# Performance work log

Measured on AMD Instinct MI355X. Metric: run time of the kernel, lower is better.

## Reference

```python
import jax, jax.numpy as jnp
import numpy as np

N, E, C, H0, H1 = 100_000, 1_600_000, 32, 128, 64


def _sage(x, src, dst, wl, bl, wr, n):
    # PyG SAGEConv(aggr='min'): lin_l(min_{j in N(i)} x_j) + lin_r(x_i); lin_r has no bias.
    agg = jax.ops.segment_min(x[src], dst, num_segments=n)  # [n, d]
    # nodes with no in-edges: PyG fills with 0 (segment_min yields dtype max)
    agg = jnp.where(agg >= jnp.finfo(x.dtype).max, jnp.zeros((), x.dtype), agg)
    return agg @ wl + bl + x @ wr


def _bn(x, g, b, eps=1e-5):
    # training-mode BatchNorm over the node dimension
    mu = jnp.mean(x, axis=0)
    var = jnp.var(x, axis=0)
    return (x - mu) * jax.lax.rsqrt(var + eps) * g + b


def _forward(x, edge_index,
             rm1_wl, rm1_bl, rm1_wr, rmn1_g, rmn1_b,
             rm2_wl, rm2_bl, rm2_wr, rmn2_g, rmn2_b,
             rm4_wl, rm4_bl, rm4_wr,
             sh1_wl, sh1_bl, sh1_wr, shn1_g, shn1_b,
             rt1_wl, rt1_bl, rt1_wr, rtn1_g, rtn1_b, rt3_w, rt3_b,
             md1_wl, md1_bl, md1_wr, mdn1_g, mdn1_b, md3_w, md3_b):
    n = x.shape[0]
    src, dst = edge_index[0], edge_index[1]
    rm = jax.nn.relu(_bn(_sage(x, src, dst, rm1_wl, rm1_bl, rm1_wr, n), rmn1_g, rmn1_b))
    rm = jax.nn.relu(_bn(_sage(rm, src, dst, rm2_wl, rm2_bl, rm2_wr, n), rmn2_g, rmn2_b))
    rm = _sage(rm, src, dst, rm4_wl, rm4_bl, rm4_wr, n)  # [n, 3]
    xs = jnp.concatenate([x, rm], axis=1)  # [n, C+3]
    xs = jax.nn.relu(_bn(_sage(xs, src, dst, sh1_wl, sh1_bl, sh1_wr, n), shn1_g, shn1_b))
    rm_ls = jax.nn.log_softmax(rm, axis=1)
    labels = (jnp.argmax(rm_ls, axis=1) == 2).astype(x.dtype)  # [n]
    rt = jax.nn.relu(_bn(_sage(xs, src, dst, rt1_wl, rt1_bl, rt1_wr, n), rtn1_g, rtn1_b))
    rt = (rt @ rt3_w + rt3_b).ravel() * labels
    md = jax.nn.relu(_bn(_sage(xs, src, dst, md1_wl, md1_bl, md1_wr, n), mdn1_g, mdn1_b))
    md = (md @ md3_w + md3_b).ravel() * labels
    return rm_ls, rt, md


def setup_inputs() -> dict:
    key = jax.random.key(0)
    ks = iter(jax.random.split(key, 64))

    def w(shape):
        s = 1.0 / np.sqrt(shape[0])
        return jax.random.uniform(next(ks), shape, jnp.float32, -s, s)

    inp = {
        "x": jax.random.normal(next(ks), (N, C), jnp.float32),
        "edge_index": jax.random.randint(next(ks), (2, E), 0, N, dtype=jnp.int32),
    }

    def sage_params(cin, cout, name):
        inp[name + "_wl"] = w((cin, cout))
        inp[name + "_bl"] = jnp.zeros((cout,), jnp.float32)
        inp[name + "_wr"] = w((cin, cout))

    def bn_params(c, name):
        inp[name + "_g"] = jnp.ones((c,), jnp.float32)
        inp[name + "_b"] = jnp.zeros((c,), jnp.float32)

    sage_params(C, H0, "rm1"); bn_params(H0, "rmn1")
    sage_params(H0, H1, "rm2"); bn_params(H1, "rmn2")
    sage_params(H1, 3, "rm4")
    sage_params(C + 3, H0, "sh1"); bn_params(H0, "shn1")
    sage_params(H0, H1, "rt1"); bn_params(H1, "rtn1")
    inp["rt3_w"] = w((H1, 1)); inp["rt3_b"] = jnp.zeros((1,), jnp.float32)
    sage_params(H0, H1, "md1"); bn_params(H1, "mdn1")
    inp["md3_w"] = w((H1, 1)); inp["md3_b"] = jnp.zeros((1,), jnp.float32)
    return inp


def reference(x, edge_index,
              rm1_wl, rm1_bl, rm1_wr, rmn1_g, rmn1_b,
              rm2_wl, rm2_bl, rm2_wr, rmn2_g, rmn2_b,
              rm4_wl, rm4_bl, rm4_wr,
              sh1_wl, sh1_bl, sh1_wr, shn1_g, shn1_b,
              rt1_wl, rt1_bl, rt1_wr, rtn1_g, rtn1_b, rt3_w, rt3_b,
              md1_wl, md1_bl, md1_wr, mdn1_g, mdn1_b, md3_w, md3_b):
    return _forward(x, edge_index,
                    rm1_wl, rm1_bl, rm1_wr, rmn1_g, rmn1_b,
                    rm2_wl, rm2_bl, rm2_wr, rmn2_g, rmn2_b,
                    rm4_wl, rm4_bl, rm4_wr,
                    sh1_wl, sh1_bl, sh1_wr, shn1_g, shn1_b,
                    rt1_wl, rt1_bl, rt1_wr, rtn1_g, rtn1_b, rt3_w, rt3_b,
                    md1_wl, md1_bl, md1_wr, mdn1_g, mdn1_b, md3_w, md3_b)
```

## Files before the change

### kernel.cpp

```cpp
#include <hip/hip_runtime.h>

#define FLTMAX 3.402823466e+38f
#define DEV __device__ __forceinline__

typedef unsigned short u16;
typedef unsigned int u32;
typedef __bf16 bf16_t;
typedef bf16_t bf16x8 __attribute__((ext_vector_type(8)));
typedef float f32x4 __attribute__((ext_vector_type(4)));

union U16x8 { uint4 u; bf16x8 b; };

DEV float trf(float v, float a, float b) { return fmaxf(fmaf(v, a, b), 0.f); }

DEV u16 f2bf(float f) {
    u32 u = __float_as_uint(f);
    return (u16)((u + 0x7FFFu + ((u >> 16) & 1u)) >> 16);
}

__global__ __launch_bounds__(256) void hist_k(const int* __restrict__ dst,
                                              int* __restrict__ deg, int E) {
    int e = blockIdx.x * 256 + threadIdx.x;
    if (e >= E) return;
    atomicAdd(&deg[dst[e]], 1);
}

__global__ __launch_bounds__(256) void scan_block_k(const int* __restrict__ deg,
                                                    int* __restrict__ ptr,
                                                    int* __restrict__ bsum, int n) {
    __shared__ int ls[256];
    int i = blockIdx.x * 256 + threadIdx.x;
    int v = (i < n) ? deg[i] : 0;
    ls[threadIdx.x] = v;
    __syncthreads();
#pragma unroll
    for (int off = 1; off < 256; off <<= 1) {
        int a = (threadIdx.x >= off) ? ls[threadIdx.x - off] : 0;
        __syncthreads();
        ls[threadIdx.x] += a;
        __syncthreads();
    }
    if (i < n) ptr[i] = ls[threadIdx.x] - v;
    if (threadIdx.x == 255) bsum[blockIdx.x] = ls[255];
}

__global__ __launch_bounds__(512) void scan_bsum_k(int* __restrict__ bsum, int nb) {
    __shared__ int ls[512];
    int t = threadIdx.x;
    int v = (t < nb) ? bsum[t] : 0;
    ls[t] = v;
    __syncthreads();
#pragma unroll
    for (int off = 1; off < 512; off <<= 1) {
        int a = (t >= off) ? ls[t - off] : 0;
        __syncthreads();
        ls[t] += a;
        __syncthreads();
    }
    if (t < nb) bsum[t] = ls[t] - v;
}

__global__ __launch_bounds__(256) void scan_add_k(int* __restrict__ ptr,
                                                  int* __restrict__ pos,
                                                  const int* __restrict__ bsum,
                                                  int n, int E) {
    int i = blockIdx.x * 256 + threadIdx.x;
    if (i == 0) ptr[n] = E;
    if (i < n) {
        int p = ptr[i] + bsum[blockIdx.x];
        ptr[i] = p;
        pos[i] = p;
    }
}

__global__ __launch_bounds__(256) void csr_fill_part_k(
    const int* __restrict__ src, const int* __restrict__ dst,
    int* __restrict__ pos, int* __restrict__ csr, int E, int lo_step) {
    const int part = blockIdx.x & 7;
    const int e = (blockIdx.x >> 3) * 256 + threadIdx.x;
    if (e >= E) return;
    const int d = dst[e];
    const int lo = part * lo_step;
    const int hi = lo + lo_step;
    if (d < lo || d >= hi) return;
    const int p = atomicAdd(&pos[d], 1);
    csr[p] = src[e];
}

__global__ __launch_bounds__(256) void gather_min32_k(
    const float* __restrict__ feat, const int* __restrict__ ptr,
    const int* __restrict__ csr, float* __restrict__ agg, int n) {
    const int lane = threadIdx.x & 63;
    const int wave = (blockIdx.x * 256 + threadIdx.x) >> 6;
    const int node = wave * 2 + (lane >> 5);
    if (node >= n) return;
    const int fl = lane & 31;
    int e = ptr[node];
    const int end = ptr[node + 1];
    const bool empty = (e == end);
    float m = FLTMAX;
    for (; e + 7 < end; e += 8) {
        int s[8];
#pragma unroll
        for (int j = 0; j < 8; j++) s[j] = csr[e + j];
        float v[8];
#pragma unroll
        for (int j = 0; j < 8; j++) v[j] = feat[(size_t)s[j] * 32 + fl];
#pragma unroll
        for (int j = 0; j < 8; j++) m = fminf(m, v[j]);
    }
    for (; e < end; e++) m = fminf(m, feat[(size_t)csr[e] * 32 + fl]);
    agg[(size_t)node * 32 + fl] = empty ? 0.f : m;
}

__global__ __launch_bounds__(256) void gather_min128_k(
    const float* __restrict__ feat, const int* __restrict__ ptr,
    const int* __restrict__ csr, const float* __restrict__ coef,
    float* __restrict__ agg, int n) {
    const int lane = threadIdx.x & 63;
    const int node = (blockIdx.x * 256 + threadIdx.x) >> 6;
    if (node >= n) return;
    const int fl = lane * 2;
    const float ca0 = coef[fl], ca1 = coef[fl + 1];
    const float cb0 = coef[128 + fl], cb1 = coef[128 + fl + 1];
    int e = ptr[node];
    const int end = ptr[node + 1];
    const bool empty = (e == end);
    float m0 = FLTMAX, m1 = FLTMAX;
    for (; e + 7 < end; e += 8) {
        int s[8];
#pragma unroll
        for (int j = 0; j < 8; j++) s[j] = csr[e + j];
        float2 v[8];
#pragma unroll
        for (int j = 0; j < 8; j++) v[j] = *(const float2*)(feat + (size_t)s[j] * 128 + fl);
#pragma unroll
        for (int j = 0; j < 8; j++) {
            m0 = fminf(m0, trf(v[j].x, ca0, cb0));
            m1 = fminf(m1, trf(v[j].y, ca1, cb1));
        }
    }
    for (; e + 3 < end; e += 4) {
        int s[4];
#pragma unroll
        for (int j = 0; j < 4; j++) s[j] = csr[e + j];
        float2 v[4];
#pragma unroll
        for (int j = 0; j < 4; j++) v[j] = *(const float2*)(feat + (size_t)s[j] * 128 + fl);
#pragma unroll
        for (int j = 0; j < 4; j++) {
            m0 = fminf(m0, trf(v[j].x, ca0, cb0));
            m1 = fminf(m1, trf(v[j].y, ca1, cb1));
        }
    }
    for (; e < end; e++) {
        const float2 v = *(const float2*)(feat + (size_t)csr[e] * 128 + fl);
        m0 = fminf(m0, trf(v.x, ca0, cb0));
        m1 = fminf(m1, trf(v.y, ca1, cb1));
    }
    float2 o;
    o.x = empty ? 0.f : m0;
    o.y = empty ? 0.f : m1;
    *(float2*)(agg + (size_t)node * 128 + fl) = o;
}

__global__ __launch_bounds__(256) void gather_bf_k(
    u16* __restrict__ Acat, const int* __restrict__ ptr,
    const int* __restrict__ csr, int n) {
    const int lane = threadIdx.x & 63;
    const int node = (blockIdx.x * 256 + threadIdx.x) >> 6;
    if (node >= n) return;
    const int fl = lane * 2;
    int e = ptr[node];
    const int end = ptr[node + 1];
    u32 outv = 0;
    if (e != end) {
        float m0 = FLTMAX, m1 = FLTMAX;
        for (; e + 15 < end; e += 16) {
            int s[16];
#pragma unroll
            for (int j = 0; j < 16; j++) s[j] = csr[e + j];
            u32 v[16];
#pragma unroll
            for (int j = 0; j < 16; j++) v[j] = *(const u32*)(Acat + (size_t)s[j] * 256 + 128 + fl);
#pragma unroll
            for (int j = 0; j < 16; j++) {
                m0 = fminf(m0, __uint_as_float(v[j] << 16));
                m1 = fminf(m1, __uint_as_float(v[j] & 0xffff0000u));
            }
        }
        for (; e + 3 < end; e += 4) {
            int s[4];
#pragma unroll
            for (int j = 0; j < 4; j++) s[j] = csr[e + j];
            u32 v[4];
#pragma unroll
            for (int j = 0; j < 4; j++) v[j] = *(const u32*)(Acat + (size_t)s[j] * 256 + 128 + fl);
#pragma unroll
            for (int j = 0; j < 4; j++) {
                m0 = fminf(m0, __uint_as_float(v[j] << 16));
                m1 = fminf(m1, __uint_as_float(v[j] & 0xffff0000u));
            }
        }
        for (; e < end; e++) {
            u32 v = *(const u32*)(Acat + (size_t)csr[e] * 256 + 128 + fl);
            m0 = fminf(m0, __uint_as_float(v << 16));
            m1 = fminf(m1, __uint_as_float(v & 0xffff0000u));
        }
        outv = (__float_as_uint(m0) >> 16) | (__float_as_uint(m1) & 0xffff0000u);
    }
    *(u32*)(Acat + (size_t)node * 256 + fl) = outv;
}

__global__ __launch_bounds__(256) void gather_min3_k(
    const float* __restrict__ feat, const int* __restrict__ ptr,
    const int* __restrict__ csr, float* __restrict__ agg, int n) {
    int i = blockIdx.x * 256 + threadIdx.x;
    if (i >= n) return;
    int e = ptr[i], end = ptr[i + 1];
    bool empty = (e == end);
    float m0 = FLTMAX, m1 = FLTMAX, m2 = FLTMAX;
    for (; e < end; e++) {
        const float* r = feat + (size_t)csr[e] * 3;
        m0 = fminf(m0, r[0]);
        m1 = fminf(m1, r[1]);
        m2 = fminf(m2, r[2]);
    }
    agg[(size_t)i * 3 + 0] = empty ? 0.f : m0;
    agg[(size_t)i * 3 + 1] = empty ? 0.f : m1;
    agg[(size_t)i * 3 + 2] = empty ? 0.f : m2;
}

__global__ __launch_bounds__(256) void convert_k(
    const float* __restrict__ h, const float* __restrict__ coef,
    u16* __restrict__ Acat, int n) {
    int t = blockIdx.x * 256 + threadIdx.x;
    int total = n * 32;
    if (t >= total) return;
    int i = t >> 5;
    int dq = (t & 31) * 4;
    const float4 hv = *(const float4*)(h + (size_t)i * 128 + dq);
    const float4 ca = *(const float4*)(coef + dq);
    const float4 cb = *(const float4*)(coef + 128 + dq);
    ushort4 o;
    o.x = f2bf(trf(hv.x, ca.x, cb.x));
    o.y = f2bf(trf(hv.y, ca.y, cb.y));
    o.z = f2bf(trf(hv.z, ca.z, cb.z));
    o.w = f2bf(trf(hv.w, ca.w, cb.w));
    *(ushort4*)(Acat + (size_t)i * 256 + 128 + dq) = o;
}

__global__ __launch_bounds__(256) void wprep_k(
    const float* __restrict__ wl, const float* __restrict__ wr,
    u16* __restrict__ WT, int N) {
    int t = blockIdx.x * 256 + threadIdx.x;
    if (t >= N * 256) return;
    int c = t >> 8;
    int k = t & 255;
    float v = (k < 128) ? wl[k * N + c] : wr[(k - 128) * N + c];
    WT[(size_t)c * 256 + k] = f2bf(v);
}

__global__ __launch_bounds__(256) void gemm_bf_k(
    const u16* __restrict__ A, const u16* __restrict__ WT,
    const float* __restrict__ bl1, const float* __restrict__ bl2,
    float* __restrict__ out, int n) {
    constexpr int NT = 8;
    const int tid = threadIdx.x;
    const int wave = tid >> 6, lane = tid & 63;
    const int quad = lane >> 4, l16 = lane & 15;
    const int row0 = blockIdx.x * 64 + wave * 16;
    const int rowA = min(row0 + l16, n - 1);
    const uint4* Arow = (const uint4*)(A + (size_t)rowA * 256) + quad;

    bf16x8 a[8];
#pragma unroll
    for (int kc = 0; kc < 8; kc++) {
        U16x8 u; u.u = Arow[kc * 4];
        a[kc] = u.b;
    }
    f32x4 acc[NT];
#pragma unroll
    for (int i = 0; i < NT; i++) acc[i] = (f32x4){0.f, 0.f, 0.f, 0.f};
#pragma unroll
    for (int nt = 0; nt < NT; nt++) {
        const uint4* Brow = (const uint4*)(WT + (size_t)(nt * 16 + l16) * 256) + quad;
#pragma unroll
        for (int kc = 0; kc < 8; kc++) {
            U16x8 u; u.u = Brow[kc * 4];
            acc[nt] = __builtin_amdgcn_mfma_f32_16x16x32_bf16(a[kc], u.b, acc[nt], 0, 0, 0);
        }
    }
#pragma unroll
    for (int nt = 0; nt < NT; nt++) {
        const int col = nt * 16 + l16;
        const float bias = (col < 64) ? bl1[col] : bl2[col - 64];
#pragma unroll
        for (int r = 0; r < 4; r++) {
            const int row = row0 + quad * 4 + r;
            if (row < n) out[(size_t)row * 128 + col] = acc[nt][r] + bias;
        }
    }
}

__global__ __launch_bounds__(256) void linear1s_k(
    const float* __restrict__ agg, const float* __restrict__ h,
    const float* __restrict__ wl, const float* __restrict__ bl,
    const float* __restrict__ wr, float* __restrict__ out, int n) {
    constexpr int DOUT = 128, CT = 32, RB = 32, LDW = 36;
    __shared__ float Ash[RB * LDW];
    __shared__ float Hsh[RB * LDW];
    const int tid = threadIdx.x;
    const int base = blockIdx.x * RB;
    {
        const int sr = tid >> 3;
        const int col = (tid & 7) * 4;
        const int grow = min(base + sr, n - 1);
        *(float4*)(Ash + sr * LDW + col) = *(const float4*)(agg + (size_t)grow * 32 + col);
        *(float4*)(Hsh + sr * LDW + col) = *(const float4*)(h + (size_t)grow * 32 + col);
    }
    __syncthreads();
    const int ct = tid % CT;
    const int rt = tid / CT;
    const int col = ct * 4;
    const int row0 = base + rt * 4;
    float4 acc[4] = {};
#pragma unroll 2
    for (int k0 = 0; k0 < 32; k0 += 4) {
        float4 wlv[4], wrv[4];
#pragma unroll
        for (int j = 0; j < 4; j++) {
            wlv[j] = *(const float4*)(wl + (size_t)(k0 + j) * DOUT + col);
            wrv[j] = *(const float4*)(wr + (size_t)(k0 + j) * DOUT + col);
        }
#pragma unroll
        for (int r = 0; r < 4; r++) {
            const float4 av = *(const float4*)(Ash + (rt * 4 + r) * LDW + k0);
            const float4 hv = *(const float4*)(Hsh + (rt * 4 + r) * LDW + k0);
#pragma unroll
            for (int j = 0; j < 4; j++) {
                const float aa = j == 0 ? av.x : j == 1 ? av.y : j == 2 ? av.z : av.w;
                const float bb = j == 0 ? hv.x : j == 1 ? hv.y : j == 2 ? hv.z : hv.w;
                acc[r].x += aa * wlv[j].x + bb * wrv[j].x;
                acc[r].y += aa * wlv[j].y + bb * wrv[j].y;
                acc[r].z += aa * wlv[j].z + bb * wrv[j].z;
                acc[r].w += aa * wlv[j].w + bb * wrv[j].w;
            }
        }
    }
    const float4 bv = *(const float4*)(bl + col);
#pragma unroll
    for (int r = 0; r < 4; r++) {
        if (row0 + r < n) {
            float4 o = acc[r];
            o.x += bv.x; o.y += bv.y; o.z += bv.z; o.w += bv.w;
            *(float4*)(out + (size_t)(row0 + r) * DOUT + col) = o;
        }
    }
}

__global__ __launch_bounds__(256) void linear2_k(
    const float* __restrict__ agg, const float* __restrict__ h,
    const float* __restrict__ coef, const float* __restrict__ wl,
    const float* __restrict__ bl, const float* __restrict__ wr,
    float* __restrict__ out, int n) {
    constexpr int DIN = 128, DOUT = 64, CT = 16, RB = 64, LDW = 132;
    __shared__ float Ash[RB * LDW];
    __shared__ float Hsh[RB * LDW];
    const int tid = threadIdx.x;
    const int base = blockIdx.x * RB;
    {
        const int sr = tid >> 2;
        const int sc = tid & 3;
        const int grow = min(base + sr, n - 1);
        const float* ar = agg + (size_t)grow * DIN;
        const float* hr = h + (size_t)grow * DIN;
#pragma unroll
        for (int c = 0; c < 8; c++) {
            const int col = (sc + c * 4) * 4;
            const float4 av = *(const float4*)(ar + col);
            float4 hv = *(const float4*)(hr + col);
            const float4 ca = *(const float4*)(coef + col);
            const float4 cb = *(const float4*)(coef + DIN + col);
            hv.x = trf(hv.x, ca.x, cb.x); hv.y = trf(hv.y, ca.y, cb.y);
            hv.z = trf(hv.z, ca.z, cb.z); hv.w = trf(hv.w, ca.w, cb.w);
            *(float4*)(Ash + sr * LDW + col) = av;
            *(float4*)(Hsh + sr * LDW + col) = hv;
        }
    }
    __syncthreads();
    const int ct = tid % CT;
    const int rt = tid / CT;
    const int col = ct * 4;
    const int row0 = base + rt * 4;
    float4 acc[4] = {};
#pragma unroll 2
    for (int k0 = 0; k0 < DIN; k0 += 4) {
        float4 wlv[4], wrv[4];
#pragma unroll
        for (int j = 0; j < 4; j++) {
            wlv[j] = *(const float4*)(wl + (size_t)(k0 + j) * DOUT + col);
            wrv[j] = *(const float4*)(wr + (size_t)(k0 + j) * DOUT + col);
        }
#pragma unroll
        for (int r = 0; r < 4; r++) {
            const float4 av = *(const float4*)(Ash + (rt * 4 + r) * LDW + k0);
            const float4 hv = *(const float4*)(Hsh + (rt * 4 + r) * LDW + k0);
#pragma unroll
            for (int j = 0; j < 4; j++) {
                const float aa = j == 0 ? av.x : j == 1 ? av.y : j == 2 ? av.z : av.w;
                const float bb = j == 0 ? hv.x : j == 1 ? hv.y : j == 2 ? hv.z : hv.w;
                acc[r].x += aa * wlv[j].x + bb * wrv[j].x;
                acc[r].y += aa * wlv[j].y + bb * wrv[j].y;
                acc[r].z += aa * wlv[j].z + bb * wrv[j].z;
                acc[r].w += aa * wlv[j].w + bb * wrv[j].w;
            }
        }
    }
    const float4 bv = *(const float4*)(bl + col);
#pragma unroll
    for (int r = 0; r < 4; r++) {
        if (row0 + r < n) {
            float4 o = acc[r];
            o.x += bv.x; o.y += bv.y; o.z += bv.z; o.w += bv.w;
            *(float4*)(out + (size_t)(row0 + r) * DOUT + col) = o;
        }
    }
}

__global__ __launch_bounds__(256) void linear_shs_k(
    const float* __restrict__ aggx, const float* __restrict__ x,
    const float* __restrict__ aggr, const float* __restrict__ rm,
    const float* __restrict__ wl, const float* __restrict__ bl,
    const float* __restrict__ wr, float* __restrict__ out, int n) {
    constexpr int DOUT = 128, CT = 32, RB = 32, LDW = 36;
    __shared__ float Ash[RB * LDW];
    __shared__ float Hsh[RB * LDW];
    __shared__ float Rsh[RB * 4], Msh[RB * 4];
    const int tid = threadIdx.x;
    const int base = blockIdx.x * RB;
    {
        const int sr = tid >> 3;
        const int col = (tid & 7) * 4;
        const int grow = min(base + sr, n - 1);
        *(float4*)(Ash + sr * LDW + col) = *(const float4*)(aggx + (size_t)grow * 32 + col);
        *(float4*)(Hsh + sr * LDW + col) = *(const float4*)(x + (size_t)grow * 32 + col);
        if (tid < RB) {
            const int gr = min(base + tid, n - 1);
#pragma unroll
            for (int k = 0; k < 3; k++) {
                Rsh[tid * 4 + k] = aggr[(size_t)gr * 3 + k];
                Msh[tid * 4 + k] = rm[(size_t)gr * 3 + k];
            }
        }
    }
    __syncthreads();
    const int ct = tid % CT;
    const int rt = tid / CT;
    const int col = ct * 4;
    const int row0 = base + rt * 4;
    float4 acc[4] = {};
#pragma unroll 2
    for (int k0 = 0; k0 < 32; k0 += 4) {
        float4 wlv[4], wrv[4];
#pragma unroll
        for (int j = 0; j < 4; j++) {
            wlv[j] = *(const float4*)(wl + (size_t)(k0 + j) * DOUT + col);
            wrv[j] = *(const float4*)(wr + (size_t)(k0 + j) * DOUT + col);
        }
#pragma unroll
        for (int r = 0; r < 4; r++) {
            const float4 av = *(const float4*)(Ash + (rt * 4 + r) * LDW + k0);
            const float4 hv = *(const float4*)(Hsh + (rt * 4 + r) * LDW + k0);
#pragma unroll
            for (int j = 0; j < 4; j++) {
                const float aa = j == 0 ? av.x : j == 1 ? av.y : j == 2 ? av.z : av.w;
                const float bb = j == 0 ? hv.x : j == 1 ? hv.y : j == 2 ? hv.z : hv.w;
                acc[r].x += aa * wlv[j].x + bb * wrv[j].x;
                acc[r].y += aa * wlv[j].y + bb * wrv[j].y;
                acc[r].z += aa * wlv[j].z + bb * wrv[j].z;
                acc[r].w += aa * wlv[j].w + bb * wrv[j].w;
            }
        }
    }
#pragma unroll
    for (int k = 0; k < 3; k++) {
        const float4 wlv = *(const float4*)(wl + (size_t)(32 + k) * DOUT + col);
        const float4 wrv = *(const float4*)(wr + (size_t)(32 + k) * DOUT + col);
#pragma unroll
        for (int r = 0; r < 4; r++) {
            const float a = Rsh[(rt * 4 + r) * 4 + k];
            const float b = Msh[(rt * 4 + r) * 4 + k];
            acc[r].x += a * wlv.x + b * wrv.x;
            acc[r].y += a * wlv.y + b * wrv.y;
            acc[r].z += a * wlv.z + b * wrv.z;
            acc[r].w += a * wlv.w + b * wrv.w;
        }
    }
    const float4 bv = *(const float4*)(bl + col);
#pragma unroll
    for (int r = 0; r < 4; r++) {
        if (row0 + r < n) {
            float4 o = acc[r];
            o.x += bv.x; o.y += bv.y; o.z += bv.z; o.w += bv.w;
            *(float4*)(out + (size_t)(row0 + r) * DOUT + col) = o;
        }
    }
}

template <int D>
__global__ __launch_bounds__(256) void colstats_k(
    const float* __restrict__ x, float* __restrict__ stats, int total) {
    __shared__ float ls[256];
    int t0 = blockIdx.x * 256 + threadIdx.x;
    int stride = gridDim.x * 256;
    float s = 0.f, s2 = 0.f;
    for (int t = t0; t < total; t += stride) {
        float v = x[t];
        s += v;
        s2 += v * v;
    }
    int col = threadIdx.x % D;
    ls[threadIdx.x] = s;
    __syncthreads();
    if (threadIdx.x < D) {
        float a = s;
        for (int u = threadIdx.x + D; u < 256; u += D) a += ls[u];
        atomicAdd(&stats[col], a);
    }
    __syncthreads();
    ls[threadIdx.x] = s2;
    __syncthreads();
    if (threadIdx.x < D) {
        float a = s2;
        for (int u = threadIdx.x + D; u < 256; u += D) a += ls[u];
        atomicAdd(&stats[D + col], a);
    }
}

template <int D>
__global__ void coef_k(const float* __restrict__ stats, const float* __restrict__ g,
                       const float* __restrict__ bb, float* __restrict__ coef,
                       float invN) {
    int d = threadIdx.x;
    if (d >= D) return;
    float mu = stats[d] * invN;
    float var = stats[D + d] * invN - mu * mu;
    float a = rsqrtf(var + 1e-5f) * g[d];
    coef[d] = a;
    coef[D + d] = bb[d] - mu * a;
}

__global__ void coef_dual_k(const float* __restrict__ stats,
                            const float* __restrict__ gR, const float* __restrict__ bR,
                            const float* __restrict__ gM, const float* __restrict__ bM,
                            float* __restrict__ coefR, float* __restrict__ coefM,
                            float invN) {
    int d = threadIdx.x;
    if (d >= 128) return;
    float mu = stats[d] * invN;
    float var = stats[128 + d] * invN - mu * mu;
    bool isR = d < 64;
    int c = isR ? d : d - 64;
    float g = isR ? gR[c] : gM[c];
    float be = isR ? bR[c] : bM[c];
    float a = rsqrtf(var + 1e-5f) * g;
    float* co = isR ? coefR : coefM;
    co[c] = a;
    co[64 + c] = be - mu * a;
}

__global__ __launch_bounds__(256) void rm_fused_k(
    const float* __restrict__ h2, const float* __restrict__ coef,
    const int* __restrict__ ptr, const int* __restrict__ csr,
    const float* __restrict__ wl, const float* __restrict__ bl,
    const float* __restrict__ wr, float* __restrict__ rmb,
    float* __restrict__ ls_out, float* __restrict__ lab, int n) {
    const int lane = threadIdx.x & 63;
    const int node = (blockIdx.x * 256 + threadIdx.x) >> 6;
    if (node >= n) return;
    const float a = coef[lane], b = coef[64 + lane];
    int e = ptr[node];
    const int end = ptr[node + 1];
    const bool empty = (e == end);
    float m = FLTMAX;
    for (; e + 15 < end; e += 16) {
        int s[16];
#pragma unroll
        for (int j = 0; j < 16; j++) s[j] = csr[e + j];
        float v[16];
#pragma unroll
        for (int j = 0; j < 16; j++) v[j] = h2[(size_t)s[j] * 64 + lane];
#pragma unroll
        for (int j = 0; j < 16; j++) m = fminf(m, trf(v[j], a, b));
    }
    for (; e + 3 < end; e += 4) {
        int s[4];
#pragma unroll
        for (int j = 0; j < 4; j++) s[j] = csr[e + j];
        float v[4];
#pragma unroll
        for (int j = 0; j < 4; j++) v[j] = h2[(size_t)s[j] * 64 + lane];
#pragma unroll
        for (int j = 0; j < 4; j++) m = fminf(m, trf(v[j], a, b));
    }
    for (; e < end; e++) m = fminf(m, trf(h2[(size_t)csr[e] * 64 + lane], a, b));
    m = empty ? 0.f : m;
    const float hv = trf(h2[(size_t)node * 64 + lane], a, b);
    float c0 = m * wl[lane * 3 + 0] + hv * wr[lane * 3 + 0];
    float c1 = m * wl[lane * 3 + 1] + hv * wr[lane * 3 + 1];
    float c2 = m * wl[lane * 3 + 2] + hv * wr[lane * 3 + 2];
#pragma unroll
    for (int off = 1; off < 64; off <<= 1) {
        c0 += __shfl_xor(c0, off);
        c1 += __shfl_xor(c1, off);
        c2 += __shfl_xor(c2, off);
    }
    const float r0 = c0 + bl[0], r1 = c1 + bl[1], r2 = c2 + bl[2];
    if (lane < 3) {
        const float r = lane == 0 ? r0 : lane == 1 ? r1 : r2;
        rmb[(size_t)node * 3 + lane] = r;
        const float mx = fmaxf(r0, fmaxf(r1, r2));
        const float lse = mx + logf(expf(r0 - mx) + expf(r1 - mx) + expf(r2 - mx));
        ls_out[(size_t)node * 3 + lane] = r - lse;
        if (lane == 0) lab[node] = (r2 > r0 && r2 > r1) ? 1.f : 0.f;
    }
}

__global__ __launch_bounds__(256) void final_k(
    const float* __restrict__ rtmd,
    const float* __restrict__ cR, const float* __restrict__ cM,
    const float* __restrict__ rtw, const float* __restrict__ rtb,
    const float* __restrict__ mdw, const float* __restrict__ mdb,
    const float* __restrict__ lab, float* __restrict__ out_rt,
    float* __restrict__ out_md, int n) {
    int i = blockIdx.x * 256 + threadIdx.x;
    if (i >= n) return;
    const float* rr = rtmd + (size_t)i * 128;
    const float* mr = rr + 64;
    float a = rtb[0], b = mdb[0];
#pragma unroll 8
    for (int k = 0; k < 64; k++) {
        a += trf(rr[k], cR[k], cR[64 + k]) * rtw[k];
        b += trf(mr[k], cM[k], cM[64 + k]) * mdw[k];
    }
    float l = lab[i];
    out_rt[i] = a * l;
    out_md[i] = b * l;
}

extern "C" void kernel_launch(void* const* d_in, const int* in_sizes, int n_in,
                              void* d_out, int out_size, void* d_ws, size_t ws_size,
                              hipStream_t stream) {
    const float* x = (const float*)d_in[0];
    const int* ei = (const int*)d_in[1];
    const int E = in_sizes[1] / 2;
    const int n = in_sizes[0] / 32;
    const int* src = ei;
    const int* dst = ei + E;

    const float* rm1_wl = (const float*)d_in[2];
    const float* rm1_bl = (const float*)d_in[3];
    const float* rm1_wr = (const float*)d_in[4];
    const float* rmn1_g = (const float*)d_in[5];
    const float* rmn1_b = (const float*)d_in[6];
    const float* rm2_wl = (const float*)d_in[7];
    const float* rm2_bl = (const float*)d_in[8];
    const float* rm2_wr = (const float*)d_in[9];
    const float* rmn2_g = (const float*)d_in[10];
    const float* rmn2_b = (const float*)d_in[11];
    const float* rm4_wl = (const float*)d_in[12];
    const float* rm4_bl = (const float*)d_in[13];
    const float* rm4_wr = (const float*)d_in[14];
    const float* sh1_wl = (const float*)d_in[15];
    const float* sh1_bl = (const float*)d_in[16];
    const float* sh1_wr = (const float*)d_in[17];
    const float* shn1_g = (const float*)d_in[18];
    const float* shn1_b = (const float*)d_in[19];
    const float* rt1_wl = (const float*)d_in[20];
    const float* rt1_bl = (const float*)d_in[21];
    const float* rt1_wr = (const float*)d_in[22];
    const float* rtn1_g = (const float*)d_in[23];
    const float* rtn1_b = (const float*)d_in[24];
    const float* rt3_w = (const float*)d_in[25];
    const float* rt3_b = (const float*)d_in[26];
    const float* md1_wl = (const float*)d_in[27];
    const float* md1_bl = (const float*)d_in[28];
    const float* md1_wr = (const float*)d_in[29];
    const float* mdn1_g = (const float*)d_in[30];
    const float* mdn1_b = (const float*)d_in[31];
    const float* md3_w = (const float*)d_in[32];
    const float* md3_b = (const float*)d_in[33];

    char* w = (char*)d_ws;
    float* aggX  = (float*)w; w += (size_t)n * 32 * 4;
    float* h1    = (float*)w; w += (size_t)n * 128 * 4;
    char*  shbuf = w;         w += (size_t)n * 512;
    float* h2rt  = (float*)w; w += (size_t)n * 128 * 4;
    float* rmb   = (float*)w; w += (size_t)n * 3 * 4;
    float* aggR  = (float*)w; w += (size_t)n * 3 * 4;
    float* lab   = (float*)w; w += (size_t)n * 4;
    float* stats = (float*)w; w += 1024 * 4;
    float* coef  = (float*)w; w += 1024 * 4;
    u16*   WTD   = (u16*)w;   w += (size_t)128 * 256 * 2;
    int* ptr  = (int*)w; w += (size_t)(n + 1) * 4;
    int* pos  = (int*)w; w += (size_t)n * 4;
    int* bsum = (int*)w; w += 1024 * 4;
    int* csr  = (int*)w; w += (size_t)E * 4;

    float* aggB = (float*)shbuf;
    u16*   Acat = (u16*)shbuf;
    float* h2 = h2rt;
    float* rtmd = h2rt;
    float* stats1 = stats, *stats2 = stats + 256, *statsSh = stats + 512, *statsD = stats + 768;
    float* coef1 = coef, *coef2 = coef + 256, *coefSh = coef + 384;
    float* coefRt = coef + 640, *coefMd = coef + 768;

    float* out = (float*)d_out;
    float* out_ls = out;
    float* out_rt = out + (size_t)3 * n;
    float* out_md = out + (size_t)4 * n;

    const float invN = 1.f / (float)n;
    auto cdiv = [](int a, int b) { return (a + b - 1) / b; };
    const int nb = cdiv(n, 256);

    hipMemsetAsync(stats, 0, 1024 * 4, stream);
    hipMemsetAsync(pos, 0, (size_t)n * 4, stream);

    hist_k<<<cdiv(E, 256), 256, 0, stream>>>(dst, pos, E);
    wprep_k<<<64, 256, 0, stream>>>(rt1_wl, rt1_wr, WTD, 64);
    wprep_k<<<64, 256, 0, stream>>>(md1_wl, md1_wr, WTD + (size_t)64 * 256, 64);
    scan_block_k<<<nb, 256, 0, stream>>>(pos, ptr, bsum, n);
    scan_bsum_k<<<1, 512, 0, stream>>>(bsum, nb);
    scan_add_k<<<nb, 256, 0, stream>>>(ptr, pos, bsum, n, E);
    csr_fill_part_k<<<cdiv(E, 256) * 8, 256, 0, stream>>>(src, dst, pos, csr, E, cdiv(n, 8));

    gather_min32_k<<<cdiv(n, 8), 256, 0, stream>>>(x, ptr, csr, aggX, n);
    linear1s_k<<<cdiv(n, 32), 256, 0, stream>>>(aggX, x, rm1_wl, rm1_bl, rm1_wr, h1, n);
    colstats_k<128><<<256, 256, 0, stream>>>(h1, stats1, n * 128);
    coef_k<128><<<1, 128, 0, stream>>>(stats1, rmn1_g, rmn1_b, coef1, invN);

    gather_min128_k<<<cdiv(n, 4), 256, 0, stream>>>(h1, ptr, csr, coef1, aggB, n);
    linear2_k<<<cdiv(n, 64), 256, 0, stream>>>(aggB, h1, coef1, rm2_wl, rm2_bl, rm2_wr, h2, n);
    colstats_k<64><<<256, 256, 0, stream>>>(h2, stats2, n * 64);
    coef_k<64><<<1, 64, 0, stream>>>(stats2, rmn2_g, rmn2_b, coef2, invN);

    rm_fused_k<<<cdiv(n, 4), 256, 0, stream>>>(h2, coef2, ptr, csr, rm4_wl, rm4_bl, rm4_wr, rmb, out_ls, lab, n);

    gather_min3_k<<<cdiv(n, 256), 256, 0, stream>>>(rmb, ptr, csr, aggR, n);
    linear_shs_k<<<cdiv(n, 32), 256, 0, stream>>>(aggX, x, aggR, rmb, sh1_wl, sh1_bl, sh1_wr, h1, n);
    colstats_k<128><<<256, 256, 0, stream>>>(h1, statsSh, n * 128);
    coef_k<128><<<1, 128, 0, stream>>>(statsSh, shn1_g, shn1_b, coefSh, invN);

    convert_k<<<cdiv(n * 32, 256), 256, 0, stream>>>(h1, coefSh, Acat, n);
    gather_bf_k<<<cdiv(n, 4), 256, 0, stream>>>(Acat, ptr, csr, n);
    gemm_bf_k<<<cdiv(n, 64), 256, 0, stream>>>(Acat, WTD, rt1_bl, md1_bl, rtmd, n);
    colstats_k<128><<<256, 256, 0, stream>>>(rtmd, statsD, n * 128);
    coef_dual_k<<<1, 128, 0, stream>>>(statsD, rtn1_g, rtn1_b, mdn1_g, mdn1_b, coefRt, coefMd, invN);

    final_k<<<cdiv(n, 256), 256, 0, stream>>>(rtmd, coefRt, coefMd,
                                              rt3_w, rt3_b, md3_w, md3_b, lab,
                                              out_rt, out_md, n);
}
```

Measured before the change: 982.1 us.

## Fuse BN column stats into GEMM epilogues, defer affine in min-gathers, parallelize final

Result: faster. 873.7 us (-11.0%).

```diff
diff --git a/kernel.cpp b/kernel.cpp
--- a/kernel.cpp
+++ b/kernel.cpp
@@ -12,6 +12,11 @@
 union U16x8 { uint4 u; bf16x8 b; };
 
 DEV float trf(float v, float a, float b) { return fmaxf(fmaf(v, a, b), 0.f); }
+
+DEV float sfmin(float m, float v, u32 sm) {
+    return fminf(m, __uint_as_float(__float_as_uint(v) ^ sm));
+}
+DEV float sdec(float m, u32 sm) { return __uint_as_float(__float_as_uint(m) ^ sm); }
 
 DEV u16 f2bf(float f) {
     u32 u = __float_as_uint(f);
@@ -123,6 +128,8 @@
     const int fl = lane * 2;
     const float ca0 = coef[fl], ca1 = coef[fl + 1];
     const float cb0 = coef[128 + fl], cb1 = coef[128 + fl + 1];
+    const u32 sm0 = (ca0 < 0.f) ? 0x80000000u : 0u;
+    const u32 sm1 = (ca1 < 0.f) ? 0x80000000u : 0u;
     int e = ptr[node];
     const int end = ptr[node + 1];
     const bool empty = (e == end);
@@ -136,8 +143,8 @@
         for (int j = 0; j < 8; j++) v[j] = *(const float2*)(feat + (size_t)s[j] * 128 + fl);
 #pragma unroll
         for (int j = 0; j < 8; j++) {
-            m0 = fminf(m0, trf(v[j].x, ca0, cb0));
-            m1 = fminf(m1, trf(v[j].y, ca1, cb1));
+            m0 = sfmin(m0, v[j].x, sm0);
+            m1 = sfmin(m1, v[j].y, sm1);
         }
     }
     for (; e + 3 < end; e += 4) {
@@ -149,18 +156,18 @@
         for (int j = 0; j < 4; j++) v[j] = *(const float2*)(feat + (size_t)s[j] * 128 + fl);
 #pragma unroll
         for (int j = 0; j < 4; j++) {
-            m0 = fminf(m0, trf(v[j].x, ca0, cb0));
-            m1 = fminf(m1, trf(v[j].y, ca1, cb1));
+            m0 = sfmin(m0, v[j].x, sm0);
+            m1 = sfmin(m1, v[j].y, sm1);
         }
     }
     for (; e < end; e++) {
         const float2 v = *(const float2*)(feat + (size_t)csr[e] * 128 + fl);
-        m0 = fminf(m0, trf(v.x, ca0, cb0));
-        m1 = fminf(m1, trf(v.y, ca1, cb1));
+        m0 = sfmin(m0, v.x, sm0);
+        m1 = sfmin(m1, v.y, sm1);
     }
     float2 o;
-    o.x = empty ? 0.f : m0;
-    o.y = empty ? 0.f : m1;
+    o.x = empty ? 0.f : trf(sdec(m0, sm0), ca0, cb0);
+    o.y = empty ? 0.f : trf(sdec(m1, sm1), ca1, cb1);
     *(float2*)(agg + (size_t)node * 128 + fl) = o;
 }
 
@@ -264,9 +271,11 @@
 __global__ __launch_bounds__(256) void gemm_bf_k(
     const u16* __restrict__ A, const u16* __restrict__ WT,
     const float* __restrict__ bl1, const float* __restrict__ bl2,
-    float* __restrict__ out, int n) {
+    float* __restrict__ out, float* __restrict__ bpart, int n) {
     constexpr int NT = 8;
+    __shared__ float bs[256];
     const int tid = threadIdx.x;
+    bs[tid] = 0.f;
     const int wave = tid >> 6, lane = tid & 63;
     const int quad = lane >> 4, l16 = lane & 15;
     const int row0 = blockIdx.x * 64 + wave * 16;
@@ -291,22 +300,34 @@
             acc[nt] = __builtin_amdgcn_mfma_f32_16x16x32_bf16(a[kc], u.b, acc[nt], 0, 0, 0);
         }
     }
+    __syncthreads();
 #pragma unroll
     for (int nt = 0; nt < NT; nt++) {
         const int col = nt * 16 + l16;
         const float bias = (col < 64) ? bl1[col] : bl2[col - 64];
+        float s = 0.f, q = 0.f;
 #pragma unroll
         for (int r = 0; r < 4; r++) {
             const int row = row0 + quad * 4 + r;
-            if (row < n) out[(size_t)row * 128 + col] = acc[nt][r] + bias;
-        }
-    }
+            if (row < n) {
+                const float o = acc[nt][r] + bias;
+                out[(size_t)row * 128 + col] = o;
+                s += o;
+                q += o * o;
+            }
+        }
+        atomicAdd(&bs[col], s);
+        atomicAdd(&bs[128 + col], q);
+    }
+    __syncthreads();
+    bpart[(size_t)blockIdx.x * 256 + tid] = bs[tid];
 }
 
 __global__ __launch_bounds__(256) void linear1s_k(
     const float* __restrict__ agg, const float* __restrict__ h,
     const float* __restrict__ wl, const float* __restrict__ bl,
-    const float* __restrict__ wr, float* __restrict__ out, int n) {
+    const float* __restrict__ wr, float* __restrict__ out,
+    float* __restrict__ bpart, int n) {
     constexpr int DOUT = 128, CT = 32, RB = 32, LDW = 36;
     __shared__ float Ash[RB * LDW];
     __shared__ float Hsh[RB * LDW];
@@ -349,12 +370,43 @@
         }
     }
     const float4 bv = *(const float4*)(bl + col);
+    float cs[4] = {}, cq[4] = {};
 #pragma unroll
     for (int r = 0; r < 4; r++) {
         if (row0 + r < n) {
             float4 o = acc[r];
             o.x += bv.x; o.y += bv.y; o.z += bv.z; o.w += bv.w;
             *(float4*)(out + (size_t)(row0 + r) * DOUT + col) = o;
+            cs[0] += o.x; cq[0] += o.x * o.x;
+            cs[1] += o.y; cq[1] += o.y * o.y;
+            cs[2] += o.z; cq[2] += o.z * o.z;
+            cs[3] += o.w; cq[3] += o.w * o.w;
+        }
+    }
+    __syncthreads();
+#pragma unroll
+    for (int j = 0; j < 4; j++) Ash[tid * 4 + j] = cs[j];
+    __syncthreads();
+    if (tid < CT) {
+#pragma unroll
+        for (int j = 0; j < 4; j++) {
+            float s = 0.f;
+#pragma unroll
+            for (int k = 0; k < 8; k++) s += Ash[(tid + k * CT) * 4 + j];
+            bpart[(size_t)blockIdx.x * 256 + tid * 4 + j] = s;
+        }
+    }
+    __syncthreads();
+#pragma unroll
+    for (int j = 0; j < 4; j++) Ash[tid * 4 + j] = cq[j];
+    __syncthreads();
+    if (tid < CT) {
+#pragma unroll
+        for (int j = 0; j < 4; j++) {
+            float s = 0.f;
+#pragma unroll
+            for (int k = 0; k < 8; k++) s += Ash[(tid + k * CT) * 4 + j];
+            bpart[(size_t)blockIdx.x * 256 + 128 + tid * 4 + j] = s;
         }
     }
 }
@@ -363,7 +415,7 @@
     const float* __restrict__ agg, const float* __restrict__ h,
     const float* __restrict__ coef, const float* __restrict__ wl,
     const float* __restrict__ bl, const float* __restrict__ wr,
-    float* __restrict__ out, int n) {
+    float* __restrict__ out, float* __restrict__ bpart, int n) {
     constexpr int DIN = 128, DOUT = 64, CT = 16, RB = 64, LDW = 132;
     __shared__ float Ash[RB * LDW];
     __shared__ float Hsh[RB * LDW];
@@ -418,12 +470,43 @@
         }
     }
     const float4 bv = *(const float4*)(bl + col);
+    float cs[4] = {}, cq[4] = {};
 #pragma unroll
     for (int r = 0; r < 4; r++) {
         if (row0 + r < n) {
             float4 o = acc[r];
             o.x += bv.x; o.y += bv.y; o.z += bv.z; o.w += bv.w;
             *(float4*)(out + (size_t)(row0 + r) * DOUT + col) = o;
+            cs[0] += o.x; cq[0] += o.x * o.x;
+            cs[1] += o.y; cq[1] += o.y * o.y;
+            cs[2] += o.z; cq[2] += o.z * o.z;
+            cs[3] += o.w; cq[3] += o.w * o.w;
+        }
+    }
+    __syncthreads();
+#pragma unroll
+    for (int j = 0; j < 4; j++) Ash[tid * 4 + j] = cs[j];
+    __syncthreads();
+    if (tid < CT) {
+#pragma unroll
+        for (int j = 0; j < 4; j++) {
+            float s = 0.f;
+#pragma unroll
+            for (int k = 0; k < 16; k++) s += Ash[(tid + k * CT) * 4 + j];
+            bpart[(size_t)blockIdx.x * 128 + tid * 4 + j] = s;
+        }
+    }
+    __syncthreads();
+#pragma unroll
+    for (int j = 0; j < 4; j++) Ash[tid * 4 + j] = cq[j];
+    __syncthreads();
+    if (tid < CT) {
+#pragma unroll
+        for (int j = 0; j < 4; j++) {
+            float s = 0.f;
+#pragma unroll
+            for (int k = 0; k < 16; k++) s += Ash[(tid + k * CT) * 4 + j];
+            bpart[(size_t)blockIdx.x * 128 + 64 + tid * 4 + j] = s;
         }
     }
 }
@@ -432,7 +515,8 @@
     const float* __restrict__ aggx, const float* __restrict__ x,
     const float* __restrict__ aggr, const float* __restrict__ rm,
     const float* __restrict__ wl, const float* __restrict__ bl,
-    const float* __restrict__ wr, float* __restrict__ out, int n) {
+    const float* __restrict__ wr, float* __restrict__ out,
+    float* __restrict__ bpart, int n) {
     constexpr int DOUT = 128, CT = 32, RB = 32, LDW = 36;
     __shared__ float Ash[RB * LDW];
     __shared__ float Hsh[RB * LDW];
@@ -498,44 +582,56 @@
         }
     }
     const float4 bv = *(const float4*)(bl + col);
+    float cs[4] = {}, cq[4] = {};
 #pragma unroll
     for (int r = 0; r < 4; r++) {
         if (row0 + r < n) {
             float4 o = acc[r];
             o.x += bv.x; o.y += bv.y; o.z += bv.z; o.w += bv.w;
             *(float4*)(out + (size_t)(row0 + r) * DOUT + col) = o;
-        }
-    }
-}
-
-template <int D>
-__global__ __launch_bounds__(256) void colstats_k(
-    const float* __restrict__ x, float* __restrict__ stats, int total) {
-    __shared__ float ls[256];
-    int t0 = blockIdx.x * 256 + threadIdx.x;
-    int stride = gridDim.x * 256;
-    float s = 0.f, s2 = 0.f;
-    for (int t = t0; t < total; t += stride) {
-        float v = x[t];
-        s += v;
-        s2 += v * v;
-    }
-    int col = threadIdx.x % D;
-    ls[threadIdx.x] = s;
-    __syncthreads();
-    if (threadIdx.x < D) {
-        float a = s;
-        for (int u = threadIdx.x + D; u < 256; u += D) a += ls[u];
-        atomicAdd(&stats[col], a);
-    }
-    __syncthreads();
-    ls[threadIdx.x] = s2;
-    __syncthreads();
-    if (threadIdx.x < D) {
-        float a = s2;
-        for (int u = threadIdx.x + D; u < 256; u += D) a += ls[u];
-        atomicAdd(&stats[D + col], a);
-    }
+            cs[0] += o.x; cq[0] += o.x * o.x;
+            cs[1] += o.y; cq[1] += o.y * o.y;
+            cs[2] += o.z; cq[2] += o.z * o.z;
+            cs[3] += o.w; cq[3] += o.w * o.w;
+        }
+    }
+    __syncthreads();
+#pragma unroll
+    for (int j = 0; j < 4; j++) Ash[tid * 4 + j] = cs[j];
+    __syncthreads();
+    if (tid < CT) {
+#pragma unroll
+        for (int j = 0; j < 4; j++) {
+            float s = 0.f;
+#pragma unroll
+            for (int k = 0; k < 8; k++) s += Ash[(tid + k * CT) * 4 + j];
+            bpart[(size_t)blockIdx.x * 256 + tid * 4 + j] = s;
+        }
+    }
+    __syncthreads();
+#pragma unroll
+    for (int j = 0; j < 4; j++) Ash[tid * 4 + j] = cq[j];
+    __syncthreads();
+    if (tid < CT) {
+#pragma unroll
+        for (int j = 0; j < 4; j++) {
+            float s = 0.f;
+#pragma unroll
+            for (int k = 0; k < 8; k++) s += Ash[(tid + k * CT) * 4 + j];
+            bpart[(size_t)blockIdx.x * 256 + 128 + tid * 4 + j] = s;
+        }
+    }
+}
+
+__global__ __launch_bounds__(256) void reduce_part_k(
+    const float* __restrict__ bpart, float* __restrict__ stats,
+    int nb, int width) {
+    const int c = threadIdx.x;
+    if (c >= width) return;
+    float s = 0.f;
+    for (int k = blockIdx.x; k < nb; k += gridDim.x)
+        s += bpart[(size_t)k * width + c];
+    atomicAdd(&stats[c], s);
 }
 
 template <int D>
@@ -580,6 +676,7 @@
     const int node = (blockIdx.x * 256 + threadIdx.x) >> 6;
     if (node >= n) return;
     const float a = coef[lane], b = coef[64 + lane];
+    const u32 sm = (a < 0.f) ? 0x80000000u : 0u;
     int e = ptr[node];
     const int end = ptr[node + 1];
     const bool empty = (e == end);
@@ -592,7 +689,7 @@
 #pragma unroll
         for (int j = 0; j < 16; j++) v[j] = h2[(size_t)s[j] * 64 + lane];
 #pragma unroll
-        for (int j = 0; j < 16; j++) m = fminf(m, trf(v[j], a, b));
+        for (int j = 0; j < 16; j++) m = sfmin(m, v[j], sm);
     }
     for (; e + 3 < end; e += 4) {
         int s[4];
@@ -602,14 +699,14 @@
 #pragma unroll
         for (int j = 0; j < 4; j++) v[j] = h2[(size_t)s[j] * 64 + lane];
 #pragma unroll
-        for (int j = 0; j < 4; j++) m = fminf(m, trf(v[j], a, b));
-    }
-    for (; e < end; e++) m = fminf(m, trf(h2[(size_t)csr[e] * 64 + lane], a, b));
-    m = empty ? 0.f : m;
+        for (int j = 0; j < 4; j++) m = sfmin(m, v[j], sm);
+    }
+    for (; e < end; e++) m = sfmin(m, h2[(size_t)csr[e] * 64 + lane], sm);
+    const float mv = empty ? 0.f : trf(sdec(m, sm), a, b);
     const float hv = trf(h2[(size_t)node * 64 + lane], a, b);
-    float c0 = m * wl[lane * 3 + 0] + hv * wr[lane * 3 + 0];
-    float c1 = m * wl[lane * 3 + 1] + hv * wr[lane * 3 + 1];
-    float c2 = m * wl[lane * 3 + 2] + hv * wr[lane * 3 + 2];
+    float c0 = mv * wl[lane * 3 + 0] + hv * wr[lane * 3 + 0];
+    float c1 = mv * wl[lane * 3 + 1] + hv * wr[lane * 3 + 1];
+    float c2 = mv * wl[lane * 3 + 2] + hv * wr[lane * 3 + 2];
 #pragma unroll
     for (int off = 1; off < 64; off <<= 1) {
         c0 += __shfl_xor(c0, off);
@@ -634,19 +731,22 @@
     const float* __restrict__ mdw, const float* __restrict__ mdb,
     const float* __restrict__ lab, float* __restrict__ out_rt,
     float* __restrict__ out_md, int n) {
-    int i = blockIdx.x * 256 + threadIdx.x;
-    if (i >= n) return;
-    const float* rr = rtmd + (size_t)i * 128;
-    const float* mr = rr + 64;
-    float a = rtb[0], b = mdb[0];
-#pragma unroll 8
-    for (int k = 0; k < 64; k++) {
-        a += trf(rr[k], cR[k], cR[64 + k]) * rtw[k];
-        b += trf(mr[k], cM[k], cM[64 + k]) * mdw[k];
-    }
-    float l = lab[i];
-    out_rt[i] = a * l;
-    out_md[i] = b * l;
+    const int lane = threadIdx.x & 63;
+    const int node = (blockIdx.x * 256 + threadIdx.x) >> 6;
+    if (node >= n) return;
+    const float* rr = rtmd + (size_t)node * 128;
+    float a = trf(rr[lane], cR[lane], cR[64 + lane]) * rtw[lane];
+    float b = trf(rr[64 + lane], cM[lane], cM[64 + lane]) * mdw[lane];
+#pragma unroll
+    for (int off = 1; off < 64; off <<= 1) {
+        a += __shfl_xor(a, off);
+        b += __shfl_xor(b, off);
+    }
+    if (lane == 0) {
+        const float l = lab[node];
+        out_rt[node] = (a + rtb[0]) * l;
+        out_md[node] = (b + mdb[0]) * l;
+    }
 }
 
 extern "C" void kernel_launch(void* const* d_in, const int* in_sizes, int n_in,
@@ -716,6 +816,11 @@
     float* coef1 = coef, *coef2 = coef + 256, *coefSh = coef + 384;
     float* coefRt = coef + 640, *coefMd = coef + 768;
 
+    float* bp1  = (float*)shbuf;
+    float* bp2  = rmb;
+    float* bpSh = (float*)shbuf;
+    float* bpD  = rmb;
+
     float* out = (float*)d_out;
     float* out_ls = out;
     float* out_rt = out + (size_t)3 * n;
@@ -724,6 +829,8 @@
     const float invN = 1.f / (float)n;
     auto cdiv = [](int a, int b) { return (a + b - 1) / b; };
     const int nb = cdiv(n, 256);
+    const int nb32 = cdiv(n, 32);
+    const int nb64 = cdiv(n, 64);
 
     hipMemsetAsync(stats, 0, 1024 * 4, stream);
     hipMemsetAsync(pos, 0, (size_t)n * 4, stream);
@@ -737,29 +844,29 @@
     csr_fill_part_k<<<cdiv(E, 256) * 8, 256, 0, stream>>>(src, dst, pos, csr, E, cdiv(n, 8));
 
     gather_min32_k<<<cdiv(n, 8), 256, 0, stream>>>(x, ptr, csr, aggX, n);
-    linear1s_k<<<cdiv(n, 32), 256, 0, stream>>>(aggX, x, rm1_wl, rm1_bl, rm1_wr, h1, n);
-    colstats_k<128><<<256, 256, 0, stream>>>(h1, stats1, n * 128);
+    linear1s_k<<<nb32, 256, 0, stream>>>(aggX, x, rm1_wl, rm1_bl, rm1_wr, h1, bp1, n);
+    reduce_part_k<<<64, 256, 0, stream>>>(bp1, stats1, nb32, 256);
     coef_k<128><<<1, 128, 0, stream>>>(stats1, rmn1_g, rmn1_b, coef1, invN);
 
     gather_min128_k<<<cdiv(n, 4), 256, 0, stream>>>(h1, ptr, csr, coef1, aggB, n);
-    linear2_k<<<cdiv(n, 64), 256, 0, stream>>>(aggB, h1, coef1, rm2_wl, rm2_bl, rm2_wr, h2, n);
-    colstats_k<64><<<256, 256, 0, stream>>>(h2, stats2, n * 64);
+    linear2_k<<<nb64, 256, 0, stream>>>(aggB, h1, coef1, rm2_wl, rm2_bl, rm2_wr, h2, bp2, n);
+    reduce_part_k<<<64, 256, 0, stream>>>(bp2, stats2, nb64, 128);
     coef_k<64><<<1, 64, 0, stream>>>(stats2, rmn2_g, rmn2_b, coef2, invN);
 
     rm_fused_k<<<cdiv(n, 4), 256, 0, stream>>>(h2, coef2, ptr, csr, rm4_wl, rm4_bl, rm4_wr, rmb, out_ls, lab, n);
 
     gather_min3_k<<<cdiv(n, 256), 256, 0, stream>>>(rmb, ptr, csr, aggR, n);
-    linear_shs_k<<<cdiv(n, 32), 256, 0, stream>>>(aggX, x, aggR, rmb, sh1_wl, sh1_bl, sh1_wr, h1, n);
-    colstats_k<128><<<256, 256, 0, stream>>>(h1, statsSh, n * 128);
+    linear_shs_k<<<nb32, 256, 0, stream>>>(aggX, x, aggR, rmb, sh1_wl, sh1_bl, sh1_wr, h1, bpSh, n);
+    reduce_part_k<<<64, 256, 0, stream>>>(bpSh, statsSh, nb32, 256);
     coef_k<128><<<1, 128, 0, stream>>>(statsSh, shn1_g, shn1_b, coefSh, invN);
 
     convert_k<<<cdiv(n * 32, 256), 256, 0, stream>>>(h1, coefSh, Acat, n);
     gather_bf_k<<<cdiv(n, 4), 256, 0, stream>>>(Acat, ptr, csr, n);
-    gemm_bf_k<<<cdiv(n, 64), 256, 0, stream>>>(Acat, WTD, rt1_bl, md1_bl, rtmd, n);
-    colstats_k<128><<<256, 256, 0, stream>>>(rtmd, statsD, n * 128);
+    gemm_bf_k<<<nb64, 256, 0, stream>>>(Acat, WTD, rt1_bl, md1_bl, rtmd, bpD, n);
+    reduce_part_k<<<64, 256, 0, stream>>>(bpD, statsD, nb64, 256);
     coef_dual_k<<<1, 128, 0, stream>>>(statsD, rtn1_g, rtn1_b, mdn1_g, mdn1_b, coefRt, coefMd, invN);
 
-    final_k<<<cdiv(n, 256), 256, 0, stream>>>(rtmd, coefRt, coefMd,
-                                              rt3_w, rt3_b, md3_w, md3_b, lab,
-                                              out_rt, out_md, n);
-}
+    final_k<<<cdiv(n, 4), 256, 0, stream>>>(rtmd, coefRt, coefMd,
+                                            rt3_w, rt3_b, md3_w, md3_b, lab,
+                                            out_rt, out_md, n);
+}
```
